# Kernel optimization log

Hardware: AMD Instinct MI355X
Metric: run time of the kernel (lower is better)

The kernel has to match this reference:

```python
import jax, jax.numpy as jnp
import numpy as np

WRITE_IDX = 123  # stand-in for tf.random.uniform scalar index (deterministic for reference)


def lqa(x, w9):
    # LearnedQuantumActivation, deterministic (training=False) path:
    # softmax-weighted blend of 8 activations + a zero 'linear' branch.
    wt = jax.nn.softmax(w9)
    mish = x * jnp.tanh(jax.nn.softplus(x))
    return (wt[0] * jax.nn.sigmoid(x) + wt[1] * jax.nn.elu(x) + wt[2] * jnp.tanh(x)
            + wt[3] * jax.nn.relu(x) + wt[4] * jax.nn.silu(x)
            + wt[5] * jax.nn.gelu(x, approximate=False) + wt[6] * jax.nn.selu(x)
            + wt[7] * mish)  # wt[8] * 0.0 (linear branch is literal 0.0)


def setup_inputs() -> dict:
    key = jax.random.key(0)
    ks = jax.random.split(key, 16)
    B, D, U, K, M, Dm = 16384, 512, 1024, 4, 4096, 512
    s = 0.05
    inp = {
        'x': jax.random.normal(ks[0], (B, D), jnp.float32),
        # DynamicPlasticDenseDendritic params
        'w': jax.random.normal(ks[1], (D, U, K), jnp.float32) * s,
        'b': jnp.zeros((U, K), jnp.float32),
        'delay': jax.random.normal(ks[2], (D, U, K), jnp.float32) * s,
        'gate_w': jax.random.normal(ks[3], (D, K), jnp.float32) * s,
        'gate_b': jnp.zeros((K,), jnp.float32),
        # LearnedQuantumActivation weights (main + the one inside DynamicConnectivity)
        'act_w_main': jnp.ones((9,), jnp.float32),
        'act_w_dc': jnp.ones((9,), jnp.float32),
        # DynamicConnectivity attention_net: Dense(U->32, LQA), Dense(32->U, sigmoid)
        'dc_w1': jax.random.normal(ks[4], (U, 32), jnp.float32) * s,
        'dc_b1': jnp.zeros((32,), jnp.float32),
        'dc_w2': jax.random.normal(ks[5], (32, U), jnp.float32) * s,
        'dc_b2': jnp.zeros((U,), jnp.float32),
        # non-trainable state
        'neuron_avg': jax.random.normal(ks[6], (U,), jnp.float32) * 0.1,
        'neuron_mask': jnp.concatenate([jnp.ones((768,), jnp.float32), jnp.zeros((U - 768,), jnp.float32)]),
        # EpisodicMemory: read Dense(U->M, softmax), write Dense(U->Dm, tanh), memory [M, Dm]
        'em_read_w': jax.random.normal(ks[7], (U, M), jnp.float32) * s,
        'em_read_b': jnp.zeros((M,), jnp.float32),
        'em_write_w': jax.random.normal(ks[8], (U, Dm), jnp.float32) * s,
        'em_write_b': jnp.zeros((Dm,), jnp.float32),
        'memory': jax.random.normal(ks[9], (M, Dm), jnp.float32) * s,
    }
    return inp


def reference(x, w, b, delay, gate_w, gate_b, act_w_main, act_w_dc,
              dc_w1, dc_b1, dc_w2, dc_b2, neuron_avg, neuron_mask,
              em_read_w, em_read_b, em_write_w, em_write_b, memory):
    # ---- DynamicPlasticDenseDendritic ----
    w_mod = w * jax.nn.sigmoid(delay)                      # [D, U, K]
    branch = jnp.einsum('bd,duk->buk', x, w_mod) + b       # [B, U, K]
    gate = jax.nn.softmax(x @ gate_w + gate_b, axis=-1)    # [B, K]
    z = jnp.einsum('buk,bk->bu', branch, gate)             # [B, U]
    # DynamicConnectivity on running neuron activation average
    h = lqa(neuron_avg[None, :] @ dc_w1 + dc_b1, act_w_dc)  # [1, 32]
    conn = jax.nn.sigmoid(h @ dc_w2 + dc_b2)                # [1, U]
    z_mod = z * conn * neuron_mask[None, :]
    a = lqa(z_mod, act_w_main)                              # [B, U]
    # ---- EpisodicMemory ----
    attention = jax.nn.softmax(a @ em_read_w + em_read_b, axis=-1)  # [B, M]
    read_vector = attention @ memory                                # [B, Dm]
    write_vector = jnp.tanh(a @ em_write_w + em_write_b)            # [B, Dm]
    agg_write = jnp.mean(write_vector, axis=0)                      # [Dm]
    new_memory = memory.at[WRITE_IDX].set(agg_write)                # scatter write
    return read_vector, new_memory
```

## Files before the change

kernel.cpp:

```cpp
#include <hip/hip_runtime.h>
#include <stdint.h>

#define B_SZ 16384
#define D_SZ 512
#define U_SZ 1024
#define NU   768
#define M_SZ 4096
#define DM   512
#define WIDX 123

typedef __attribute__((ext_vector_type(8))) short short8;
typedef __attribute__((ext_vector_type(4))) float f32x4;
typedef __attribute__((ext_vector_type(8))) int  i32x8;

__device__ __forceinline__ unsigned short f2bf(float f){
  union { float f; unsigned int u; } v; v.f = f;
  unsigned int r = (v.u + 0x7FFFu + ((v.u >> 16) & 1u)) >> 16;
  return (unsigned short)r;
}
__device__ __forceinline__ unsigned char f2e4m3(float f){
  return (unsigned char)(__builtin_amdgcn_cvt_pk_fp8_f32(f, f, 0, 0) & 0xff);
}

__device__ __forceinline__ float lqa_f(float x, const float* wt){
  float xc = fminf(fmaxf(x, -20.f), 20.f);
  float t  = __expf(xc);
  float t2 = t * t;
  float sig = t / (1.f + t);
  float elu = x > 0.f ? x : t - 1.f;
  float th  = (t2 - 1.f) / (t2 + 1.f);
  float rel = fmaxf(x, 0.f);
  float sil = x * sig;
  float y   = xc * 0.70710678118654752f;
  float ay  = fabsf(y);
  float k   = 1.f / (1.f + 0.3275911f * ay);
  float poly = k*(0.254829592f + k*(-0.284496736f + k*(1.421413741f + k*(-1.453152027f + k*1.061405429f))));
  float er  = 1.f - poly * __expf(-y * y);
  er = y < 0.f ? -er : er;
  float gel = 0.5f * x * (1.f + er);
  float sel = 1.0507009873554805f * (x > 0.f ? x : 1.6732632423543772f * (t - 1.f));
  float ms  = t2 + 2.f * t;
  float mis = x * ms / (ms + 2.f);
  return wt[0]*sig + wt[1]*elu + wt[2]*th + wt[3]*rel
       + wt[4]*sil + wt[5]*gel + wt[6]*sel + wt[7]*mis;
}

__global__ __launch_bounds__(256) void prep_kernel(
    const float* __restrict__ awm, const float* __restrict__ awdc,
    const float* __restrict__ dc_w1, const float* __restrict__ dc_b1,
    const float* __restrict__ dc_w2, const float* __restrict__ dc_b2,
    const float* __restrict__ navg, const float* __restrict__ nmask,
    float* __restrict__ wt_main, float* __restrict__ connmask){
  __shared__ float wtdc[9];
  __shared__ float hsh[32];
  __shared__ float nsh[U_SZ];
  int t = threadIdx.x;
  for (int i = t; i < U_SZ; i += 256) nsh[i] = navg[i];
  if (t == 0){
    float m = awm[0]; for (int i=1;i<9;i++) m = fmaxf(m, awm[i]);
    float e[9], s = 0.f;
    for (int i=0;i<9;i++){ e[i] = expf(awm[i]-m); s += e[i]; }
    for (int i=0;i<9;i++) wt_main[i] = e[i]/s;
    m = awdc[0]; for (int i=1;i<9;i++) m = fmaxf(m, awdc[i]);
    s = 0.f; for (int i=0;i<9;i++){ e[i] = expf(awdc[i]-m); s += e[i]; }
    for (int i=0;i<9;i++) wtdc[i] = e[i]/s;
  }
  __syncthreads();
  if (t < 32){
    float acc = 0.f;
    for (int u = 0; u < U_SZ; ++u) acc += nsh[u] * dc_w1[u*32 + t];
    hsh[t] = lqa_f(acc + dc_b1[t], wtdc);
  }
  __syncthreads();
  for (int u = t; u < U_SZ; u += 256){
    float c = dc_b2[u];
    for (int j = 0; j < 32; ++j) c += hsh[j] * dc_w2[j*U_SZ + u];
    connmask[u] = (1.f / (1.f + expf(-c))) * nmask[u];
  }
}

__global__ __launch_bounds__(256) void foldbias_kernel(
    const float* __restrict__ wt_main,
    const float* __restrict__ em_r_w, const float* __restrict__ em_r_b,
    const float* __restrict__ em_w_w, const float* __restrict__ em_w_b,
    float* __restrict__ cbR, float* __restrict__ cbW){
  int d = blockIdx.x*256 + threadIdx.x;
  float c0 = 0.5f * wt_main[0];
  if (d < M_SZ){
    float s = 0.f;
    for (int u = NU; u < U_SZ; ++u) s += em_r_w[(size_t)u*M_SZ + d];
    cbR[d] = em_r_b[d] + c0 * s;
  } else {
    int d2 = d - M_SZ;
    if (d2 < DM){
      float s = 0.f;
      for (int u = NU; u < U_SZ; ++u) s += em_w_w[(size_t)u*DM + d2];
      cbW[d2] = em_w_b[d2] + c0 * s;
    }
  }
}

__global__ __launch_bounds__(256) void gate_x2_kernel(
    const float* __restrict__ x, const float* __restrict__ gate_w,
    const float* __restrict__ gate_b, float* __restrict__ gate_out,
    unsigned char* __restrict__ X2_8){
  int b = blockIdx.x, t = threadIdx.x;
  int w = t >> 6, lane = t & 63;
  float2 xv = ((const float2*)(x + (size_t)b * D_SZ))[t];
  float4 g0 = ((const float4*)gate_w)[2*t];
  float4 g1 = ((const float4*)gate_w)[2*t+1];
  float p0 = xv.x*g0.x + xv.y*g1.x;
  float p1 = xv.x*g0.y + xv.y*g1.y;
  float p2 = xv.x*g0.z + xv.y*g1.z;
  float p3 = xv.x*g0.w + xv.y*g1.w;
  #pragma unroll
  for (int o = 32; o > 0; o >>= 1){
    p0 += __shfl_down(p0,o); p1 += __shfl_down(p1,o);
    p2 += __shfl_down(p2,o); p3 += __shfl_down(p3,o);
  }
  __shared__ float red[4][4];
  __shared__ float gsh[4];
  if (lane == 0){ red[w][0]=p0; red[w][1]=p1; red[w][2]=p2; red[w][3]=p3; }
  __syncthreads();
  if (t == 0){
    float l0 = red[0][0]+red[1][0]+red[2][0]+red[3][0] + gate_b[0];
    float l1 = red[0][1]+red[1][1]+red[2][1]+red[3][1] + gate_b[1];
    float l2 = red[0][2]+red[1][2]+red[2][2]+red[3][2] + gate_b[2];
    float l3 = red[0][3]+red[1][3]+red[2][3]+red[3][3] + gate_b[3];
    float m = fmaxf(fmaxf(l0,l1), fmaxf(l2,l3));
    float e0 = expf(l0-m), e1 = expf(l1-m), e2 = expf(l2-m), e3 = expf(l3-m);
    float s = e0+e1+e2+e3;
    gsh[0]=e0/s; gsh[1]=e1/s; gsh[2]=e2/s; gsh[3]=e3/s;
    float* go = gate_out + (size_t)b*4;
    go[0]=gsh[0]; go[1]=gsh[1]; go[2]=gsh[2]; go[3]=gsh[3];
  }
  __syncthreads();
  float q0=gsh[0], q1=gsh[1], q2=gsh[2], q3=gsh[3];
  const float S = 8.f;
  int w0 = __builtin_amdgcn_cvt_pk_fp8_f32(xv.x*q0*S, xv.x*q1*S, 0, 0);
  w0     = __builtin_amdgcn_cvt_pk_fp8_f32(xv.x*q2*S, xv.x*q3*S, w0, 1);
  int w1 = __builtin_amdgcn_cvt_pk_fp8_f32(xv.y*q0*S, xv.y*q1*S, 0, 0);
  w1     = __builtin_amdgcn_cvt_pk_fp8_f32(xv.y*q2*S, xv.y*q3*S, w1, 1);
  *(uint2*)(X2_8 + (size_t)b*2048 + t*8) = make_uint2((unsigned)w0, (unsigned)w1);
}

__global__ __launch_bounds__(256) void convert_wz_kernel(
    const float* __restrict__ w, const float* __restrict__ delay,
    unsigned char* __restrict__ Wzt8){
  int t = blockIdx.x*256 + threadIdx.x;
  int u = t & (U_SZ-1), d = t >> 10;
  float4 wv = ((const float4*)w)[t];
  float4 dv = ((const float4*)delay)[t];
  const float S = 32.f;
  float m0 = S * wv.x * (1.f/(1.f+__expf(-dv.x)));
  float m1 = S * wv.y * (1.f/(1.f+__expf(-dv.y)));
  float m2 = S * wv.z * (1.f/(1.f+__expf(-dv.z)));
  float m3 = S * wv.w * (1.f/(1.f+__expf(-dv.w)));
  int o = __builtin_amdgcn_cvt_pk_fp8_f32(m0, m1, 0, 0);
  o     = __builtin_amdgcn_cvt_pk_fp8_f32(m2, m3, o, 1);
  *(int*)(Wzt8 + (size_t)u*2048 + d*4) = o;
}

__global__ __launch_bounds__(256) void transpose_f32_bf16(
    const float* __restrict__ in, unsigned short* __restrict__ out, int R, int C){
  __shared__ float tile[64][65];
  int c0 = blockIdx.x*64, r0 = blockIdx.y*64;
  int t = threadIdx.x;
  int ri = t >> 2, cj = (t & 3) * 16;
  const float* src = in + (size_t)(r0+ri)*C + c0 + cj;
  #pragma unroll
  for (int i=0;i<4;i++){
    float4 v = ((const float4*)src)[i];
    tile[ri][cj+4*i+0]=v.x; tile[ri][cj+4*i+1]=v.y;
    tile[ri][cj+4*i+2]=v.z; tile[ri][cj+4*i+3]=v.w;
  }
  __syncthreads();
  int co = t >> 2, rj = (t & 3) * 16;
  unsigned int o8[8];
  #pragma unroll
  for (int i=0;i<8;i++){
    unsigned short a = f2bf(tile[rj+2*i][co]);
    unsigned short b = f2bf(tile[rj+2*i+1][co]);
    o8[i] = a | ((unsigned)b << 16);
  }
  unsigned short* dst = out + (size_t)(c0+co)*R + r0 + rj;
  ((uint4*)dst)[0] = make_uint4(o8[0],o8[1],o8[2],o8[3]);
  ((uint4*)dst)[1] = make_uint4(o8[4],o8[5],o8[6],o8[7]);
}

__global__ __launch_bounds__(256) void transpose_f32_fp8(
    const float* __restrict__ in, unsigned char* __restrict__ out,
    int ld, int C, float S){
  __shared__ float tile[64][65];
  int c0 = blockIdx.x*64, r0 = blockIdx.y*64;
  int t = threadIdx.x;
  int ri = t >> 2, cj = (t & 3) * 16;
  const float* src = in + (size_t)(r0+ri)*C + c0 + cj;
  #pragma unroll
  for (int i=0;i<4;i++){
    float4 v = ((const float4*)src)[i];
    tile[ri][cj+4*i+0]=v.x; tile[ri][cj+4*i+1]=v.y;
    tile[ri][cj+4*i+2]=v.z; tile[ri][cj+4*i+3]=v.w;
  }
  __syncthreads();
  int co = t >> 2, rj = (t & 3) * 16;
  unsigned int oi[4];
  #pragma unroll
  for (int i=0;i<4;i++){
    int v = __builtin_amdgcn_cvt_pk_fp8_f32(tile[rj+4*i+0][co]*S, tile[rj+4*i+1][co]*S, 0, 0);
    v     = __builtin_amdgcn_cvt_pk_fp8_f32(tile[rj+4*i+2][co]*S, tile[rj+4*i+3][co]*S, v, 1);
    oi[i] = (unsigned)v;
  }
  *(uint4*)(out + (size_t)(c0+co)*ld + r0 + rj) = make_uint4(oi[0],oi[1],oi[2],oi[3]);
}

__device__ __forceinline__ void gl_lds16(const unsigned short* g, unsigned short* l){
  __builtin_amdgcn_global_load_lds((const __attribute__((address_space(1))) void*)g,
      (__attribute__((address_space(3))) void*)l, 16, 0, 0);
}
__device__ __forceinline__ void gl_lds16b(const unsigned char* g, unsigned char* l){
  __builtin_amdgcn_global_load_lds((const __attribute__((address_space(1))) void*)g,
      (__attribute__((address_space(3))) void*)l, 16, 0, 0);
}

__device__ __forceinline__ void xcd_swizzle(int& mTile, int& nTile){
  int nx = gridDim.x, nwg = nx * gridDim.y;
  int orig = blockIdx.y * nx + blockIdx.x;
  int q = nwg >> 3, r = nwg & 7;
  int xcd = orig & 7, off = orig >> 3;
  int id = (xcd < r ? xcd * (q + 1) : r * (q + 1) + (xcd - r) * q) + off;
  mTile = id / nx;
  nTile = id % nx;
}

template<int EPI, unsigned SCALEA, unsigned SCALEB>
__global__ __launch_bounds__(256, 2)
void gemmF8(const unsigned char* __restrict__ A, int lda,
            const unsigned char* __restrict__ Bt, int ldb, int ntiles,
            float* __restrict__ outF, unsigned short* __restrict__ outB,
            unsigned char* __restrict__ outB8, int ldout,
            const float* __restrict__ colBias,
            const float* __restrict__ gate, const float* __restrict__ biasUK,
            const float* __restrict__ connmask, const float* __restrict__ wtp,
            float* __restrict__ rowRed)
{
  __shared__ __align__(16) unsigned char lds8[32768];
  const int tid = threadIdx.x;
  const int w = tid >> 6, lane = tid & 63;
  const int wr = w >> 1, wc = w & 1;
  const int lr = lane & 15, g4 = lane >> 4;
  int mT, nT; xcd_swizzle(mT, nT);
  const int mBase = mT * 128, nBase = nT * 128;

  f32x4 acc[4][4];
  #pragma unroll
  for (int i=0;i<4;i++)
    #pragma unroll
    for (int j=0;j<4;j++) acc[i][j] = (f32x4){0.f,0.f,0.f,0.f};

  const int srow  = w*32 + (lane >> 3);
  const int scolb = (((lane & 7) ^ ((lane >> 3) & 7)) << 4);
  const unsigned char* aS = A  + (size_t)(mBase + srow)*lda + scolb;
  const unsigned char* bS = Bt + (size_t)(nBase + srow)*ldb + scolb;

  auto RD8 = [&](int off, int R)->i32x8 {
    int x0 = off + R*128 + ((g4*32     ) ^ ((R & 7) << 4));
    int x1 = off + R*128 + ((g4*32 + 16) ^ ((R & 7) << 4));
    int4 u0 = *(const int4*)&lds8[x0];
    int4 u1 = *(const int4*)&lds8[x1];
    i32x8 r;
    r[0]=u0.x; r[1]=u0.y; r[2]=u0.z; r[3]=u0.w;
    r[4]=u1.x; r[5]=u1.y; r[6]=u1.z; r[7]=u1.w;
    return r;
  };

  for (int kt = 0; kt < ntiles; ++kt){
    __syncthreads();
    #pragma unroll
    for (int j=0;j<4;j++)
      gl_lds16b(aS + (size_t)(j*8)*lda + kt*128, &lds8[(w*32 + j*8)*128]);
    #pragma unroll
    for (int j=0;j<4;j++)
      gl_lds16b(bS + (size_t)(j*8)*ldb + kt*128, &lds8[16384 + (w*32 + j*8)*128]);
    __syncthreads();
    i32x8 af[4], bf[4];
    #pragma unroll
    for (int m=0;m<4;m++) af[m] = RD8(0,     wr*64 + m*16 + lr);
    #pragma unroll
    for (int n=0;n<4;n++) bf[n] = RD8(16384, wc*64 + n*16 + lr);
    #pragma unroll
    for (int m=0;m<4;m++)
      #pragma unroll
      for (int n=0;n<4;n++)
        acc[m][n] = __builtin_amdgcn_mfma_scale_f32_16x16x128_f8f6f4(
            af[m], bf[n], acc[m][n], 0, 0, 0, (int)SCALEA, 0, (int)SCALEB);
  }

  if constexpr (EPI == 0){
    float wtl[8];
    #pragma unroll
    for (int i=0;i<8;i++) wtl[i] = wtp[i];
    #pragma unroll
    for (int mi=0; mi<4; mi++){
      #pragma unroll
      for (int j=0;j<4;j++){
        int grr = mBase + wr*64 + mi*16 + g4*4 + j;
        float4 gv = *(const float4*)&gate[(size_t)grr*4];
        #pragma unroll
        for (int ni=0; ni<4; ni++){
          int gc = nBase + wc*64 + ni*16 + lr;
          float4 bb = *(const float4*)&biasUK[(size_t)gc*4];
          float v = acc[mi][ni][j] + gv.x*bb.x + gv.y*bb.y + gv.z*bb.z + gv.w*bb.w;
          v *= connmask[gc];
          float a = lqa_f(v, wtl);
          outB [(size_t)grr*ldout + gc] = f2bf(a);
          outB8[(size_t)grr*ldout + gc] = f2e4m3(a * 8.f);
        }
      }
    }
  } else if constexpr (EPI == 1){
    #pragma unroll
    for (int mi=0; mi<4; mi++){
      #pragma unroll
      for (int j=0;j<4;j++){
        int grr = mBase + wr*64 + mi*16 + g4*4 + j;
        float s = 0.f;
        #pragma unroll
        for (int ni=0; ni<4; ni++){
          int gc = nBase + wc*64 + ni*16 + lr;
          float p = __expf(acc[mi][ni][j] + colBias[gc]);
          outB8[(size_t)grr*ldout + gc] = f2e4m3(p * 16.f);
          s += p;
        }
        s += __shfl_xor(s, 1); s += __shfl_xor(s, 2);
        s += __shfl_xor(s, 4); s += __shfl_xor(s, 8);
        if (lr == 0) atomicAdd(&rowRed[grr], s);
      }
    }
  } else {
    #pragma unroll
    for (int mi=0; mi<4; mi++)
      #pragma unroll
      for (int j=0;j<4;j++){
        int grr = mBase + wr*64 + mi*16 + g4*4 + j;
        float dinv = 1.f / rowRed[grr];
        #pragma unroll
        for (int ni=0; ni<4; ni++){
          int gc = nBase + wc*64 + ni*16 + lr;
          outF[(size_t)grr*ldout + gc] = acc[mi][ni][j] * dinv;
        }
      }
  }
}

template<int EPI>
__global__ __launch_bounds__(256, 2)
void gemm8(const unsigned short* __restrict__ A, int lda,
           const unsigned short* __restrict__ Bt, int ldb, int ntiles,
           const float* __restrict__ colBias,
           float* __restrict__ rowRed)
{
  __shared__ __align__(16) unsigned short lds[32768];
  const int tid  = threadIdx.x;
  const int w    = tid >> 6, lane = tid & 63;
  const int wr   = w >> 1, wc = w & 1;
  const int lr   = lane & 15, g4 = lane >> 4;
  int mT, nT; xcd_swizzle(mT, nT);
  const int mBase = mT * 128, nBase = nT * 128;

  f32x4 acc[4][4];
  #pragma unroll
  for (int i=0;i<4;i++)
    #pragma unroll
    for (int j=0;j<4;j++) acc[i][j] = (f32x4){0.f,0.f,0.f,0.f};

  short8 aF[2][2], b0[2][2], b1[2][2];

  const int srow = w*16 + (lane >> 3);
  const int scol = ((lane & 7) ^ ((lane >> 3) & 7)) << 3;
  const unsigned short* aSrc = A  + (size_t)(mBase + srow)*lda + scol;
  const unsigned short* bSrc = Bt + (size_t)(nBase + srow)*ldb + scol;
  const int dstBase = w*1024;

  auto STAGE = [&](int isB, int buf, int half, int kt){
    const unsigned short* sb = isB ? bSrc : aSrc;
    const int ldx = isB ? ldb : lda;
    const int dE  = (isB ? 16384 : 0) + buf*8192 + half*4096 + dstBase;
    gl_lds16(sb + (size_t)(half*64    )*ldx + kt*64, &lds[dE      ]);
    gl_lds16(sb + (size_t)(half*64 + 8)*ldx + kt*64, &lds[dE + 512]);
  };
  auto RD = [&](int aOff, int r, int kk)->short8 {
    int e = aOff + r*64 + ((kk + g4*8) ^ ((r & 7) << 3));
    return *(const short8*)&lds[e];
  };

#define READA(QM, BUF) { _Pragma("unroll") for (int i2=0;i2<2;i2++) \
    _Pragma("unroll") for (int k2=0;k2<2;k2++) \
      aF[i2][k2] = RD((BUF)*8192, wr*64 + ((QM)*2+i2)*16 + lr, k2*32); }
#define READB(QN, BUF, BV) { _Pragma("unroll") for (int i2=0;i2<2;i2++) \
    _Pragma("unroll") for (int k2=0;k2<2;k2++) \
      BV[i2][k2] = RD(16384 + (BUF)*8192, wc*64 + ((QN)*2+i2)*16 + lr, k2*32); }
#define MFMAQ(QM, QN, BV) { \
    _Pragma("unroll") for (int i2=0;i2<2;i2++) \
    _Pragma("unroll") for (int k2=0;k2<2;k2++) \
    _Pragma("unroll") for (int j2=0;j2<2;j2++) \
      acc[(QM)*2+i2][(QN)*2+j2] = __builtin_amdgcn_mfma_f32_16x16x32_bf16( \
          aF[i2][k2], BV[j2][k2], acc[(QM)*2+i2][(QN)*2+j2], 0, 0, 0); }
#define OPENP  { __builtin_amdgcn_s_barrier(); \
                 asm volatile("s_waitcnt lgkmcnt(0)" ::: "memory"); \
                 __builtin_amdgcn_sched_barrier(0); \
                 __builtin_amdgcn_s_setprio(1); }
#define CLOSEP { __builtin_amdgcn_s_setprio(0); \
                 asm volatile("s_barrier" ::: "memory"); }

  STAGE(0,0,0,0); STAGE(0,0,1,0); STAGE(1,0,0,0); STAGE(1,0,1,0);
  STAGE(0,1,0,1); STAGE(0,1,1,1); STAGE(1,1,0,1); STAGE(1,1,1,1);
  asm volatile("s_waitcnt vmcnt(8)" ::: "memory");
  asm volatile("s_barrier" ::: "memory");

  const int NI = ntiles >> 1;
  for (int it = 0; it < NI; ++it){
    const int t1 = 2*it+1, t2 = 2*it+2, t3 = 2*it+3;
    READA(0, 0); READB(0, 0, b0); READB(1, 0, b1);
    if (it > 0){ STAGE(0, 1, 0, t1); STAGE(0, 1, 1, t1); }
    OPENP; MFMAQ(0, 0, b0); MFMAQ(0, 1, b1); CLOSEP;
    READA(1, 0);
    if (t2 < ntiles){
      STAGE(1, 0, 0, t2); STAGE(1, 0, 1, t2);
      asm volatile("s_waitcnt vmcnt(4)" ::: "memory");
    } else {
      asm volatile("s_waitcnt vmcnt(0)" ::: "memory");
    }
    OPENP; MFMAQ(1, 1, b1); MFMAQ(1, 0, b0); CLOSEP;
    READA(0, 1); READB(0, 1, b0); READB(1, 1, b1);
    if (t2 < ntiles){ STAGE(0, 0, 0, t2); STAGE(0, 0, 1, t2); }
    OPENP; MFMAQ(0, 0, b0); MFMAQ(0, 1, b1); CLOSEP;
    READA(1, 1);
    if (t3 < ntiles){ STAGE(1, 1, 0, t3); STAGE(1, 1, 1, t3); }
    asm volatile("s_waitcnt vmcnt(4)" ::: "memory");
    OPENP; MFMAQ(1, 1, b1); MFMAQ(1, 0, b0); CLOSEP;
  }

  #pragma unroll
  for (int ni=0; ni<4; ni++){
    int gc = nBase + wc*64 + ni*16 + lr;
    float cb = colBias[gc];
    float s = 0.f;
    #pragma unroll
    for (int mi=0; mi<4; mi++)
      #pragma unroll
      for (int j=0;j<4;j++){
        float v = acc[mi][ni][j] + cb;
        float vc = fminf(fmaxf(v, -15.f), 15.f);
        float e2 = __expf(2.f*vc);
        s += (e2 - 1.f) / (e2 + 1.f);
      }
    s += __shfl_xor(s, 16); s += __shfl_xor(s, 32);
    if (lane < 16) atomicAdd(&rowRed[gc], s);
  }
#undef READA
#undef READB
#undef MFMAQ
#undef OPENP
#undef CLOSEP
}

__global__ __launch_bounds__(256) void finalize_mem(
    float* __restrict__ out, const float* __restrict__ agg,
    const float* __restrict__ memory){
  size_t j = (size_t)blockIdx.x*256 + threadIdx.x;
  int row = (int)(j >> 9);
  float v = memory[j];
  if (row == WIDX) v = agg[j & 511] * (1.f / (float)B_SZ);
  out[(size_t)B_SZ*DM + j] = v;
}

extern "C" void kernel_launch(void* const* d_in, const int* in_sizes, int n_in,
                              void* d_out, int out_size, void* d_ws, size_t ws_size,
                              hipStream_t stream){
  (void)in_sizes; (void)n_in; (void)out_size; (void)ws_size;
  const float* x      = (const float*)d_in[0];
  const float* w      = (const float*)d_in[1];
  const float* bUK    = (const float*)d_in[2];
  const float* delay  = (const float*)d_in[3];
  const float* gate_w = (const float*)d_in[4];
  const float* gate_b = (const float*)d_in[5];
  const float* awm    = (const float*)d_in[6];
  const float* awdc   = (const float*)d_in[7];
  const float* dc_w1  = (const float*)d_in[8];
  const float* dc_b1  = (const float*)d_in[9];
  const float* dc_w2  = (const float*)d_in[10];
  const float* dc_b2  = (const float*)d_in[11];
  const float* navg   = (const float*)d_in[12];
  const float* nmask  = (const float*)d_in[13];
  const float* em_r_w = (const float*)d_in[14];
  const float* em_r_b = (const float*)d_in[15];
  const float* em_w_w = (const float*)d_in[16];
  const float* em_w_b = (const float*)d_in[17];
  const float* memory = (const float*)d_in[18];

  char* ws = (char*)d_ws;
  float* wt_main  = (float*)(ws + 0);
  float* connmask = (float*)(ws + 256);
  float* denom    = (float*)(ws + 4608);
  float* agg      = (float*)(ws + 70144);
  float* gate     = (float*)(ws + 72192);
  float* cbR      = (float*)(ws + 334336);
  float* cbW      = (float*)(ws + 350720);

  size_t o = 360448;
  unsigned char* Pbuf8 = (unsigned char*)(ws + o);
  unsigned char* X2_8  = Pbuf8;
  o += 67108864;
  unsigned char* Wzt8  = (unsigned char*)(ws + o); o += 2097152;
  unsigned short* abuf = (unsigned short*)(ws + o); o += 25165824;
  unsigned char* abuf8 = (unsigned char*)(ws + o); o += 12582912;
  unsigned char* Wrt8  = (unsigned char*)(ws + o); o += 4194304;
  unsigned short* Wwt  = (unsigned short*)(ws + o); o += 1048576;
  unsigned char* memT8 = (unsigned char*)(ws + o);

  hipMemsetAsync(ws + 4608, 0, 67584, stream);

  prep_kernel<<<dim3(1), dim3(256), 0, stream>>>(awm, awdc, dc_w1, dc_b1, dc_w2, dc_b2,
                                                 navg, nmask, wt_main, connmask);
  foldbias_kernel<<<dim3(18), dim3(256), 0, stream>>>(wt_main, em_r_w, em_r_b,
                                                      em_w_w, em_w_b, cbR, cbW);
  gate_x2_kernel<<<dim3(B_SZ), dim3(256), 0, stream>>>(x, gate_w, gate_b, gate, X2_8);
  convert_wz_kernel<<<dim3(2048), dim3(256), 0, stream>>>(w, delay, Wzt8);
  transpose_f32_fp8<<<dim3(M_SZ/64, U_SZ/64), dim3(256), 0, stream>>>(em_r_w, Wrt8, 1024, M_SZ, 16.f);
  transpose_f32_bf16<<<dim3(DM/64,  U_SZ/64), dim3(256), 0, stream>>>(em_w_w, Wwt, U_SZ, DM);
  transpose_f32_fp8<<<dim3(DM/64,  M_SZ/64), dim3(256), 0, stream>>>(memory, memT8, M_SZ, DM, 16.f);

  gemmF8<0, 0x7C7C7C7Cu, 0x7A7A7A7Au><<<dim3(NU/128, B_SZ/128), dim3(256), 0, stream>>>(
      X2_8, 2048, Wzt8, 2048, 16,
      nullptr, abuf, abuf8, NU, nullptr, gate, bUK, connmask, wt_main, nullptr);

  gemmF8<1, 0x7C7C7C7Cu, 0x7B7B7B7Bu><<<dim3(M_SZ/128, B_SZ/128), dim3(256), 0, stream>>>(
      abuf8, NU, Wrt8, 1024, 6,
      nullptr, nullptr, Pbuf8, 4096, cbR, nullptr, nullptr, nullptr, nullptr, denom);

  gemmF8<5, 0x7B7B7B7Bu, 0x7B7B7B7Bu><<<dim3(DM/128, B_SZ/128), dim3(256), 0, stream>>>(
      Pbuf8, 4096, memT8, 4096, 32,
      (float*)d_out, nullptr, nullptr, 512, nullptr, nullptr, nullptr, nullptr, nullptr, denom);

  gemm8<3><<<dim3(DM/128, B_SZ/128), dim3(256), 0, stream>>>(
      abuf, NU, Wwt, 1024, 12, cbW, agg);

  finalize_mem<<<dim3((M_SZ*DM)/256), dim3(256), 0, stream>>>(
      (float*)d_out, agg, memory);
}
```

Measured before the change: 317.2 us.

## Double-buffer LDS in FP8 GEMM with ping-pong MFMA/load scheduling

Doubles the FP8 GEMM's LDS to 64KB so A and B tiles are double-buffered. The K loop is restructured into quadrant-wise MFMA phases that interleave with async global-to-LDS staging of the next tiles. It uses explicit vmcnt waits, barriers and s_setprio to overlap memory with compute, replacing the sync-load-sync-compute pattern. The larger LDS footprint may lower occupancy, and the hand-tuned waitcnt choreography risks race conditions if the counts are wrong.

```diff
diff --git a/kernel.cpp b/kernel.cpp
--- a/kernel.cpp
+++ b/kernel.cpp
@@ -244,7 +244,7 @@
             const float* __restrict__ connmask, const float* __restrict__ wtp,
             float* __restrict__ rowRed)
 {
-  __shared__ __align__(16) unsigned char lds8[32768];
+  __shared__ __align__(16) unsigned char lds8[65536];
   const int tid = threadIdx.x;
   const int w = tid >> 6, lane = tid & 63;
   const int wr = w >> 1, wc = w & 1;
@@ -258,11 +258,21 @@
     #pragma unroll
     for (int j=0;j<4;j++) acc[i][j] = (f32x4){0.f,0.f,0.f,0.f};
 
-  const int srow  = w*32 + (lane >> 3);
+  i32x8 aF[2], b0[2], b1[2];
+
+  const int srow  = w*16 + (lane >> 3);
   const int scolb = (((lane & 7) ^ ((lane >> 3) & 7)) << 4);
-  const unsigned char* aS = A  + (size_t)(mBase + srow)*lda + scolb;
-  const unsigned char* bS = Bt + (size_t)(nBase + srow)*ldb + scolb;
-
+  const unsigned char* aSrc = A  + (size_t)(mBase + srow)*lda + scolb;
+  const unsigned char* bSrc = Bt + (size_t)(nBase + srow)*ldb + scolb;
+  const int dstBase = w*2048;
+
+  auto STAGE = [&](int isB, int buf, int half, int kt){
+    const unsigned char* sb = isB ? bSrc : aSrc;
+    const int ldx = isB ? ldb : lda;
+    const int dE  = (isB ? 32768 : 0) + buf*16384 + half*8192 + dstBase;
+    gl_lds16b(sb + (size_t)(half*64    )*ldx + kt*128, &lds8[dE       ]);
+    gl_lds16b(sb + (size_t)(half*64 + 8)*ldx + kt*128, &lds8[dE + 1024]);
+  };
   auto RD8 = [&](int off, int R)->i32x8 {
     int x0 = off + R*128 + ((g4*32     ) ^ ((R & 7) << 4));
     int x1 = off + R*128 + ((g4*32 + 16) ^ ((R & 7) << 4));
@@ -274,26 +284,48 @@
     return r;
   };
 
-  for (int kt = 0; kt < ntiles; ++kt){
-    __syncthreads();
-    #pragma unroll
-    for (int j=0;j<4;j++)
-      gl_lds16b(aS + (size_t)(j*8)*lda + kt*128, &lds8[(w*32 + j*8)*128]);
-    #pragma unroll
-    for (int j=0;j<4;j++)
-      gl_lds16b(bS + (size_t)(j*8)*ldb + kt*128, &lds8[16384 + (w*32 + j*8)*128]);
-    __syncthreads();
-    i32x8 af[4], bf[4];
-    #pragma unroll
-    for (int m=0;m<4;m++) af[m] = RD8(0,     wr*64 + m*16 + lr);
-    #pragma unroll
-    for (int n=0;n<4;n++) bf[n] = RD8(16384, wc*64 + n*16 + lr);
-    #pragma unroll
-    for (int m=0;m<4;m++)
-      #pragma unroll
-      for (int n=0;n<4;n++)
-        acc[m][n] = __builtin_amdgcn_mfma_scale_f32_16x16x128_f8f6f4(
-            af[m], bf[n], acc[m][n], 0, 0, 0, (int)SCALEA, 0, (int)SCALEB);
+#define READA(QM, BUF) { _Pragma("unroll") for (int i2=0;i2<2;i2++) \
+      aF[i2] = RD8((BUF)*16384, wr*64 + ((QM)*2+i2)*16 + lr); }
+#define READB(QN, BUF, BV) { _Pragma("unroll") for (int j2=0;j2<2;j2++) \
+      BV[j2] = RD8(32768 + (BUF)*16384, wc*64 + ((QN)*2+j2)*16 + lr); }
+#define MFMAQ(QM, QN, BV) { \
+    _Pragma("unroll") for (int i2=0;i2<2;i2++) \
+    _Pragma("unroll") for (int j2=0;j2<2;j2++) \
+      acc[(QM)*2+i2][(QN)*2+j2] = __builtin_amdgcn_mfma_scale_f32_16x16x128_f8f6f4( \
+          aF[i2], BV[j2], acc[(QM)*2+i2][(QN)*2+j2], 0, 0, 0, (int)SCALEA, 0, (int)SCALEB); }
+#define OPENP  { __builtin_amdgcn_s_barrier(); \
+                 asm volatile("s_waitcnt lgkmcnt(0)" ::: "memory"); \
+                 __builtin_amdgcn_sched_barrier(0); \
+                 __builtin_amdgcn_s_setprio(1); }
+#define CLOSEP { __builtin_amdgcn_s_setprio(0); \
+                 asm volatile("s_barrier" ::: "memory"); }
+
+  STAGE(0,0,0,0); STAGE(0,0,1,0); STAGE(1,0,0,0); STAGE(1,0,1,0);
+  STAGE(0,1,0,1); STAGE(0,1,1,1); STAGE(1,1,0,1); STAGE(1,1,1,1);
+  asm volatile("s_waitcnt vmcnt(8)" ::: "memory");
+  asm volatile("s_barrier" ::: "memory");
+
+  const int NI = ntiles >> 1;
+  for (int it = 0; it < NI; ++it){
+    const int t1 = 2*it+1, t2 = 2*it+2, t3 = 2*it+3;
+    READA(0, 0); READB(0, 0, b0); READB(1, 0, b1);
+    if (it > 0){ STAGE(0, 1, 0, t1); STAGE(0, 1, 1, t1); }
+    OPENP; MFMAQ(0, 0, b0); MFMAQ(0, 1, b1); CLOSEP;
+    READA(1, 0);
+    if (t2 < ntiles){
+      STAGE(1, 0, 0, t2); STAGE(1, 0, 1, t2);
+      asm volatile("s_waitcnt vmcnt(4)" ::: "memory");
+    } else {
+      asm volatile("s_waitcnt vmcnt(0)" ::: "memory");
+    }
+    OPENP; MFMAQ(1, 1, b1); MFMAQ(1, 0, b0); CLOSEP;
+    READA(0, 1); READB(0, 1, b0); READB(1, 1, b1);
+    if (t2 < ntiles){ STAGE(0, 0, 0, t2); STAGE(0, 0, 1, t2); }
+    OPENP; MFMAQ(0, 0, b0); MFMAQ(0, 1, b1); CLOSEP;
+    READA(1, 1);
+    if (t3 < ntiles){ STAGE(1, 1, 0, t3); STAGE(1, 1, 1, t3); }
+    asm volatile("s_waitcnt vmcnt(4)" ::: "memory");
+    OPENP; MFMAQ(1, 1, b1); MFMAQ(1, 0, b0); CLOSEP;
   }
 
   if constexpr (EPI == 0){
@@ -351,6 +383,11 @@
         }
       }
   }
+#undef READA
+#undef READB
+#undef MFMAQ
+#undef OPENP
+#undef CLOSEP
 }
 
 template<int EPI>
```

New measurement: 352.7 us. 11.2% more time.

## Load B fragments directly from global into registers, stage only A in LDS

Applied to the files above, without the earlier changes.

The FP8 GEMM kernel no longer stages the B tile through shared memory. Each wave now loads its B fragments straight from global memory into registers, and only A goes through LDS, which halves LDS use to 16 KB. The aim is to cut LDS traffic and footprint and possibly raise occupancy. The cost is uncoalesced, redundant global loads of B, since the two wave rows each fetch the same B columns, and global latency is exposed with no prefetch.

```diff
diff --git a/kernel.cpp b/kernel.cpp
--- a/kernel.cpp
+++ b/kernel.cpp
@@ -244,7 +244,7 @@
             const float* __restrict__ connmask, const float* __restrict__ wtp,
             float* __restrict__ rowRed)
 {
-  __shared__ __align__(16) unsigned char lds8[32768];
+  __shared__ __align__(16) unsigned char lds8[16384];
   const int tid = threadIdx.x;
   const int w = tid >> 6, lane = tid & 63;
   const int wr = w >> 1, wc = w & 1;
@@ -260,12 +260,13 @@
 
   const int srow  = w*32 + (lane >> 3);
   const int scolb = (((lane & 7) ^ ((lane >> 3) & 7)) << 4);
-  const unsigned char* aS = A  + (size_t)(mBase + srow)*lda + scolb;
-  const unsigned char* bS = Bt + (size_t)(nBase + srow)*ldb + scolb;
-
-  auto RD8 = [&](int off, int R)->i32x8 {
-    int x0 = off + R*128 + ((g4*32     ) ^ ((R & 7) << 4));
-    int x1 = off + R*128 + ((g4*32 + 16) ^ ((R & 7) << 4));
+  const unsigned char* aS = A + (size_t)(mBase + srow)*lda + scolb;
+
+  const unsigned char* bRow = Bt + (size_t)(nBase + wc*64 + lr)*ldb + g4*32;
+
+  auto RD8 = [&](int R)->i32x8 {
+    int x0 = R*128 + ((g4*32     ) ^ ((R & 7) << 4));
+    int x1 = R*128 + ((g4*32 + 16) ^ ((R & 7) << 4));
     int4 u0 = *(const int4*)&lds8[x0];
     int4 u1 = *(const int4*)&lds8[x1];
     i32x8 r;
@@ -273,27 +274,33 @@
     r[4]=u1.x; r[5]=u1.y; r[6]=u1.z; r[7]=u1.w;
     return r;
   };
+  auto LDB = [&](int n, int kt)->i32x8 {
+    const unsigned char* p = bRow + (size_t)(n*16)*ldb + kt*128;
+    int4 u0 = *(const int4*)p;
+    int4 u1 = *(const int4*)(p + 16);
+    i32x8 r;
+    r[0]=u0.x; r[1]=u0.y; r[2]=u0.z; r[3]=u0.w;
+    r[4]=u1.x; r[5]=u1.y; r[6]=u1.z; r[7]=u1.w;
+    return r;
+  };
 
   for (int kt = 0; kt < ntiles; ++kt){
+    i32x8 bf[4];
+    #pragma unroll
+    for (int n=0;n<4;n++) bf[n] = LDB(n, kt);
     __syncthreads();
     #pragma unroll
     for (int j=0;j<4;j++)
       gl_lds16b(aS + (size_t)(j*8)*lda + kt*128, &lds8[(w*32 + j*8)*128]);
-    #pragma unroll
-    for (int j=0;j<4;j++)
-      gl_lds16b(bS + (size_t)(j*8)*ldb + kt*128, &lds8[16384 + (w*32 + j*8)*128]);
     __syncthreads();
-    i32x8 af[4], bf[4];
-    #pragma unroll
-    for (int m=0;m<4;m++) af[m] = RD8(0,     wr*64 + m*16 + lr);
-    #pragma unroll
-    for (int n=0;n<4;n++) bf[n] = RD8(16384, wc*64 + n*16 + lr);
-    #pragma unroll
-    for (int m=0;m<4;m++)
+    #pragma unroll
+    for (int m=0;m<4;m++){
+      i32x8 af = RD8(wr*64 + m*16 + lr);
       #pragma unroll
       for (int n=0;n<4;n++)
         acc[m][n] = __builtin_amdgcn_mfma_scale_f32_16x16x128_f8f6f4(
-            af[m], bf[n], acc[m][n], 0, 0, 0, (int)SCALEA, 0, (int)SCALEB);
+            af, bf[n], acc[m][n], 0, 0, 0, (int)SCALEA, 0, (int)SCALEB);
+    }
   }
 
   if constexpr (EPI == 0){
```

Measured after the change: 430.0 us. 35.5% more time.
